# Performance work log

Hardware: AMD Instinct MI355X
Metric: run time of the kernel (lower is better)

The kernel has to match this reference:

```python
import jax, jax.numpy as jnp
import numpy as np

B, Q, C = 8, 100, 1024
H, W = 64, 64
NH = 16
HD = C // NH
SCALE = HD ** -0.5
LN_EPS = 1e-5


def setup_inputs() -> dict:
    key = jax.random.key(0)
    ks = jax.random.split(key, 8)
    xav = lambda k, shp: jax.random.normal(k, shp, jnp.float32) * (2.0 / (shp[0] + shp[-1])) ** 0.5
    return {
        "tgt": jax.random.normal(ks[0], (B, Q, C), jnp.float32),
        "memory": jax.random.normal(ks[1], (B, H, W, C), jnp.float32),
        "memory_pos_emb": jax.random.normal(ks[2], (B, H, W, C), jnp.float32),
        "query_pos_emb": jax.random.normal(ks[3], (B, Q, C), jnp.float32),
        "Wq": xav(ks[4], (C, C)),
        "Wk": xav(ks[5], (C, C)),
        "Wv": xav(ks[6], (C, C)),
        "Wo": xav(ks[7], (C, C)),
        "bo": jnp.zeros((C,), jnp.float32),
        "ln_gamma": jnp.ones((C,), jnp.float32),
        "ln_beta": jnp.zeros((C,), jnp.float32),
    }


def _layernorm(x, g, b):
    mu = jnp.mean(x, axis=-1, keepdims=True)
    var = jnp.var(x, axis=-1, keepdims=True)
    return (x - mu) * jax.lax.rsqrt(var + LN_EPS) * g + b


def reference(tgt, memory, memory_pos_emb, query_pos_emb, Wq, Wk, Wv, Wo, bo, ln_gamma, ln_beta):
    # flatten spatial dims: [B,H,W,C] -> [B,K,C]
    mem = memory.reshape(B, H * W, C)
    mpos = memory_pos_emb.reshape(B, H * W, C)
    q_in = tgt + query_pos_emb          # [B,Q,C]
    k_in = mem + mpos                    # [B,K,C]
    # projections (torch Linear: x @ W.T), split heads -> [B,nh,*,hd]
    q = (q_in @ Wq.T).reshape(B, Q, NH, HD).transpose(0, 2, 1, 3)
    k = (k_in @ Wk.T).reshape(B, -1, NH, HD).transpose(0, 2, 1, 3)
    v = (mem @ Wv.T).reshape(B, -1, NH, HD).transpose(0, 2, 1, 3)
    dots = jnp.einsum('bhid,bhjd->bhij', q, k) * SCALE   # [B,nh,Q,K]
    # slot attention: softmax over QUERY axis, then renormalize over keys
    attn = jax.nn.softmax(dots, axis=2)
    attn = attn / (jnp.sum(attn, axis=-1, keepdims=True) + 1e-8)
    updates = jnp.einsum('bhij,bhjd->bhid', attn, v)     # [B,nh,Q,hd]
    updates = updates.transpose(0, 2, 1, 3).reshape(B, Q, C)
    out = updates @ Wo.T + bo
    # residual (dropout is identity in eval) + post-LayerNorm
    return _layernorm(tgt + out, ln_gamma, ln_beta)
```

## Files before the change

kernel.cpp:

```cpp
#include <hip/hip_runtime.h>

typedef unsigned short u16;
typedef __attribute__((ext_vector_type(8))) short bf16x8;
typedef __attribute__((ext_vector_type(4))) short bf16x4;
typedef __attribute__((ext_vector_type(4))) float f32x4;
typedef __attribute__((ext_vector_type(4))) unsigned short u16x4;
typedef __attribute__((ext_vector_type(8))) unsigned short u16x8;
typedef __attribute__((ext_vector_type(4))) int i32x4;
typedef __attribute__((ext_vector_type(4))) float f4;

#define DI __device__ __forceinline__


DI u16 f2bf(float f){
  unsigned int u = __float_as_uint(f);
  return (u16)((u + 0x7FFFu + ((u >> 16) & 1u)) >> 16);
}

DI void gl_lds16(const void* g, void* l){
  __builtin_amdgcn_global_load_lds((const __attribute__((address_space(1))) unsigned int*)g,
                                   (__attribute__((address_space(3))) unsigned int*)l, 16, 0, 0);
}

__global__ __launch_bounds__(256) void prep_kv(const float* __restrict__ mem,
                                               const float* __restrict__ mpos,
                                               u16* __restrict__ kA, u16* __restrict__ vA){
  const int t = blockIdx.x * 256 + threadIdx.x;
  #pragma unroll
  for (int i = 0; i < 2; ++i){
    const size_t g = (size_t)t + (size_t)i * 2097152;
    f4 m0 = ((const f4*)mem)[g * 2];
    f4 m1 = ((const f4*)mem)[g * 2 + 1];
    f4 p0 = ((const f4*)mpos)[g * 2];
    f4 p1 = ((const f4*)mpos)[g * 2 + 1];
    u16x8 k, v;
    #pragma unroll
    for (int j = 0; j < 4; ++j){
      k[j]     = f2bf(m0[j] + p0[j]);  v[j]     = f2bf(m0[j]);
      k[j + 4] = f2bf(m1[j] + p1[j]);  v[j + 4] = f2bf(m1[j]);
    }
    ((u16x8*)kA)[g] = k;
    ((u16x8*)vA)[g] = v;
  }
}

__global__ __launch_bounds__(256) void prep_qw(const float* __restrict__ tgt,
                                               const float* __restrict__ qpos,
                                               const float* __restrict__ Wq, const float* __restrict__ Wk,
                                               const float* __restrict__ Wv, const float* __restrict__ Wo,
                                               u16* __restrict__ qA, u16* __restrict__ Wbf){
  int gid = blockIdx.x * 256 + threadIdx.x;
  const int NQ4 = 819200 / 4;
  if (gid < NQ4){
    f4 a = ((const f4*)tgt)[gid];
    f4 b = ((const f4*)qpos)[gid];
    u16x4 r;
    #pragma unroll
    for (int j = 0; j < 4; ++j) r[j] = f2bf(a[j] + b[j]);
    ((u16x4*)qA)[gid] = r;
  } else {
    int wid = gid - NQ4;
    int sel = wid >> 18;
    int off = wid & 262143;
    const float* W = (sel == 0) ? Wq : (sel == 1) ? Wk : (sel == 2) ? Wv : Wo;
    f4 w = ((const f4*)W)[off];
    u16x4 r;
    #pragma unroll
    for (int j = 0; j < 4; ++j) r[j] = f2bf(w[j]);
    ((u16x4*)(Wbf))[(size_t)sel * 262144 + off] = r;
  }
}

__global__ __launch_bounds__(512, 1) void gemm256(
    const u16* __restrict__ A, const u16* __restrict__ Bw,
    u16* __restrict__ Cb, float scale)
{
  __shared__ __align__(16) char lds[131072];
  const int tid = threadIdx.x;
  const int l = tid & 63, w = tid >> 6;
  const int nwg = gridDim.x;
  const int sbid = (blockIdx.x & 7) * (nwg >> 3) + (blockIdx.x >> 3);
  const int mb = sbid >> 2, nb = sbid & 3;
  const int m0 = mb * 256, n0 = nb * 256;
  const int fr = l & 15, fg = l >> 4;
  const int wm = w >> 2, wn = w & 3;

  char* ldsA  = lds + wm * 8192 + l * 16;
  char* ldsB  = lds + 32768 + wn * 4096 + l * 16;
  char* ldsS0 = lds + w * 1024;
  char* ldsS1 = lds + (8 + w) * 1024;
  const u16* gA0 = A  + (size_t)(m0 + w * 16 + fr) * 1024 + fg * 8;
  const u16* gA1 = A  + (size_t)(m0 + (8 + w) * 16 + fr) * 1024 + fg * 8;
  const u16* gB0 = Bw + (size_t)(n0 + w * 16 + fr) * 1024 + fg * 8;
  const u16* gB1 = Bw + (size_t)(n0 + (8 + w) * 16 + fr) * 1024 + fg * 8;

  auto stA = [&](int pp, int kh, int kt){
    const int o = kt * 64 + kh * 32;
    gl_lds16(gA0 + o, ldsS0 + pp * 65536 + kh * 16384);
    gl_lds16(gA1 + o, ldsS1 + pp * 65536 + kh * 16384);
  };
  auto stB = [&](int pp, int kh, int kt){
    const int o = kt * 64 + kh * 32;
    gl_lds16(gB0 + o, ldsS0 + pp * 65536 + 32768 + kh * 16384);
    gl_lds16(gB1 + o, ldsS1 + pp * 65536 + 32768 + kh * 16384);
  };
  auto rdA4 = [&](bf16x8* av, int pp, int kh, int mfb){
    #pragma unroll
    for (int i = 0; i < 4; ++i)
      av[i] = *(const bf16x8*)(ldsA + pp * 65536 + kh * 16384 + (mfb + i) * 1024);
  };
  auto rdB4 = [&](bf16x8* bv, int pp, int kh){
    #pragma unroll
    for (int i = 0; i < 4; ++i)
      bv[i] = *(const bf16x8*)(ldsB + pp * 65536 + kh * 16384 + i * 1024);
  };

  f32x4 acc[8][4] = {};

  stA(0, 0, 0); stB(0, 0, 0); stA(0, 1, 0); stB(0, 1, 0);
  stA(1, 0, 1); stB(1, 0, 1);
  asm volatile("s_waitcnt vmcnt(8)" ::: "memory");
  __builtin_amdgcn_s_barrier();

  auto ktbody = [&](int P, int kt){
    const int kt1 = (kt + 1 > 15) ? 15 : kt + 1;
    const int kt2 = (kt + 2 > 15) ? 15 : kt + 2;
    bf16x8 av[4], bv[4];

    rdA4(av, P, 0, 0); rdB4(bv, P, 0);
    stA(P ^ 1, 1, kt1);
    __builtin_amdgcn_s_barrier();
    __builtin_amdgcn_s_setprio(1);
    #pragma unroll
    for (int i = 0; i < 4; ++i)
      #pragma unroll
      for (int n = 0; n < 4; ++n)
        acc[i][n] = __builtin_amdgcn_mfma_f32_16x16x32_bf16(av[i], bv[n], acc[i][n], 0, 0, 0);
    __builtin_amdgcn_s_setprio(0);
    __builtin_amdgcn_s_barrier();

    rdA4(av, P, 0, 4);
    stB(P ^ 1, 1, kt1);
    asm volatile("s_waitcnt vmcnt(8)" ::: "memory");
    __builtin_amdgcn_s_barrier();
    __builtin_amdgcn_s_setprio(1);
    #pragma unroll
    for (int i = 0; i < 4; ++i)
      #pragma unroll
      for (int n = 0; n < 4; ++n)
        acc[4 + i][n] = __builtin_amdgcn_mfma_f32_16x16x32_bf16(av[i], bv[n], acc[4 + i][n], 0, 0, 0);
    __builtin_amdgcn_s_setprio(0);
    __builtin_amdgcn_s_barrier();

    rdA4(av, P, 1, 0); rdB4(bv, P, 1);
    stA(P, 0, kt2);
    __builtin_amdgcn_s_barrier();
    __builtin_amdgcn_s_setprio(1);
    #pragma unroll
    for (int i = 0; i < 4; ++i)
      #pragma unroll
      for (int n = 0; n < 4; ++n)
        acc[i][n] = __builtin_amdgcn_mfma_f32_16x16x32_bf16(av[i], bv[n], acc[i][n], 0, 0, 0);
    __builtin_amdgcn_s_setprio(0);
    __builtin_amdgcn_s_barrier();

    rdA4(av, P, 1, 4);
    stB(P, 0, kt2);
    asm volatile("s_waitcnt vmcnt(8)" ::: "memory");
    __builtin_amdgcn_s_barrier();
    __builtin_amdgcn_s_setprio(1);
    #pragma unroll
    for (int i = 0; i < 4; ++i)
      #pragma unroll
      for (int n = 0; n < 4; ++n)
        acc[4 + i][n] = __builtin_amdgcn_mfma_f32_16x16x32_bf16(av[i], bv[n], acc[4 + i][n], 0, 0, 0);
    __builtin_amdgcn_s_setprio(0);
    __builtin_amdgcn_s_barrier();
  };

  for (int kk = 0; kk < 8; ++kk){
    ktbody(0, 2 * kk);
    ktbody(1, 2 * kk + 1);
  }

  asm volatile("s_waitcnt vmcnt(0)" ::: "memory");

  #pragma unroll
  for (int mf = 0; mf < 8; ++mf){
    #pragma unroll
    for (int nf = 0; nf < 4; ++nf){
      const int gcol = n0 + wn * 64 + nf * 16 + fr;
      #pragma unroll
      for (int r = 0; r < 4; ++r){
        const int grow = m0 + wm * 128 + mf * 16 + fg * 4 + r;
        Cb[(size_t)grow * 1024 + gcol] = f2bf(acc[mf][nf][r] * scale);
      }
    }
  }
}

template<int MODE>
__global__ __launch_bounds__(256, 2) void gemm_bt(
    const u16* __restrict__ A, const u16* __restrict__ Bw,
    u16* __restrict__ Cb, float* __restrict__ Cf,
    const float* __restrict__ bias, const float* __restrict__ resid,
    int M, float scale)
{
  __shared__ u16 lA[2][128 * 32];
  __shared__ u16 lB[2][128 * 32];
  const int tid = threadIdx.x;
  const int l = tid & 63, w = tid >> 6;
  const int nwg = gridDim.x;
  int bid = blockIdx.x;
  bid = (bid & 7) * (nwg >> 3) + (bid >> 3);
  const int mb = bid >> 3, nb = bid & 7;
  const int m0 = mb * 128, n0 = nb * 128;
  const int fr = l & 15, fg = l >> 4;
  const int wr = w >> 1, wc = w & 1;

  f32x4 acc[4][4] = {};

  auto stage = [&](int buf, int kt){
    const int k0 = kt * 32;
    #pragma unroll
    for (int q = 0; q < 2; ++q){
      int r = w * 32 + q * 16 + (l >> 2);
      int ar = m0 + r; if (ar >= M) ar = M - 1;
      gl_lds16(A  + (size_t)ar * 1024 + k0 + (l & 3) * 8, &lA[buf][(w * 32 + q * 16) * 32]);
      gl_lds16(Bw + (size_t)(n0 + r) * 1024 + k0 + (l & 3) * 8, &lB[buf][(w * 32 + q * 16) * 32]);
    }
  };

  stage(0, 0);
  __syncthreads();
  for (int kt = 0; kt < 32; ++kt){
    const int cur = kt & 1;
    if (kt < 31) stage(cur ^ 1, kt + 1);
    bf16x8 av[4], bv[4];
    #pragma unroll
    for (int m = 0; m < 4; ++m)
      av[m] = *(const bf16x8*)&lA[cur][(wr * 64 + m * 16 + fr) * 32 + fg * 8];
    #pragma unroll
    for (int n = 0; n < 4; ++n)
      bv[n] = *(const bf16x8*)&lB[cur][(wc * 64 + n * 16 + fr) * 32 + fg * 8];
    #pragma unroll
    for (int m = 0; m < 4; ++m)
      #pragma unroll
      for (int n = 0; n < 4; ++n)
        acc[m][n] = __builtin_amdgcn_mfma_f32_16x16x32_bf16(av[m], bv[n], acc[m][n], 0, 0, 0);
    __syncthreads();
  }

  #pragma unroll
  for (int m = 0; m < 4; ++m){
    const int grow_base = m0 + wr * 64 + m * 16 + fg * 4;
    #pragma unroll
    for (int n = 0; n < 4; ++n){
      const int gcol = n0 + wc * 64 + n * 16 + fr;
      #pragma unroll
      for (int r = 0; r < 4; ++r){
        const int grow = grow_base + r;
        if (grow < M){
          const float v = acc[m][n][r];
          if (MODE == 0) Cb[(size_t)grow * 1024 + gcol] = f2bf(v * scale);
          else           Cf[(size_t)grow * 1024 + gcol] = v + bias[gcol] + resid[(size_t)grow * 1024 + gcol];
        }
      }
    }
  }
}

__global__ __launch_bounds__(64, 1) void attn_k(
    const u16* __restrict__ qp, const u16* __restrict__ kp, const u16* __restrict__ vp,
    float* __restrict__ updpart, float* __restrict__ rspart)
{
  const int bidx = blockIdx.x;
  const int c = bidx & 7, h = (bidx >> 3) & 15, b = bidx >> 7;
  const int bh = b * 16 + h;
  const int l = threadIdx.x;
  const int fr = l & 15, fg = l >> 4;

  __shared__ u16 qlds[112 * 64];
  for (int t = 0; t < 14; ++t){
    int chunk = t * 64 + l;
    int row = chunk >> 3, cb = chunk & 7;
    i32x4 val = {0, 0, 0, 0};
    if (row < 100)
      val = *(const i32x4*)(qp + (size_t)(b * 100 + row) * 1024 + h * 64 + cb * 8);
    *(i32x4*)((char*)qlds + row * 128 + ((cb ^ (row & 7)) * 16)) = val;
  }
  __syncthreads();

  bf16x8 qf[7][2];
  #pragma unroll
  for (int n = 0; n < 7; ++n)
    #pragma unroll
    for (int ks = 0; ks < 2; ++ks){
      int row = n * 16 + fr;
      int cb = ks * 4 + fg;
      qf[n][ks] = *(const bf16x8*)((const char*)qlds + row * 128 + ((cb ^ (row & 7)) * 16));
    }

  f32x4 acc[7][4] = {};
  float rs[7] = {};
  const f32x4 fz = {0.f, 0.f, 0.f, 0.f};
  const size_t kvbase = ((size_t)b * 4096) * 1024 + h * 64;

  for (int t = 0; t < 32; ++t){
    const int j0 = c * 512 + t * 16;
    bf16x8 kf0 = *(const bf16x8*)(kp + kvbase + (size_t)(j0 + fr) * 1024 + fg * 8);
    bf16x8 kf1 = *(const bf16x8*)(kp + kvbase + (size_t)(j0 + fr) * 1024 + 32 + fg * 8);
    f32x4 s[7];
    #pragma unroll
    for (int n = 0; n < 7; ++n){
      s[n] = __builtin_amdgcn_mfma_f32_16x16x32_bf16(kf0, qf[n][0], fz, 0, 0, 0);
      s[n] = __builtin_amdgcn_mfma_f32_16x16x32_bf16(kf1, qf[n][1], s[n], 0, 0, 0);
    }
    if (fr >= 4){ s[6][0] = -1e30f; s[6][1] = -1e30f; s[6][2] = -1e30f; s[6][3] = -1e30f; }

    float pv[7][4];
    #pragma unroll
    for (int r = 0; r < 4; ++r){
      float m = s[0][r];
      #pragma unroll
      for (int n = 1; n < 7; ++n) m = fmaxf(m, s[n][r]);
      m = fmaxf(m, __shfl_xor(m, 1)); m = fmaxf(m, __shfl_xor(m, 2));
      m = fmaxf(m, __shfl_xor(m, 4)); m = fmaxf(m, __shfl_xor(m, 8));
      float sum = 0.f;
      #pragma unroll
      for (int n = 0; n < 7; ++n){ float e = __expf(s[n][r] - m); pv[n][r] = e; sum += e; }
      sum += __shfl_xor(sum, 1); sum += __shfl_xor(sum, 2);
      sum += __shfl_xor(sum, 4); sum += __shfl_xor(sum, 8);
      float inv = 1.0f / sum;
      #pragma unroll
      for (int n = 0; n < 7; ++n) pv[n][r] *= inv;
    }

    bf16x4 pk[7];
    #pragma unroll
    for (int n = 0; n < 7; ++n){
      rs[n] += pv[n][0] + pv[n][1] + pv[n][2] + pv[n][3];
      bf16x4 t4;
      t4[0] = (short)f2bf(pv[n][0]); t4[1] = (short)f2bf(pv[n][1]);
      t4[2] = (short)f2bf(pv[n][2]); t4[3] = (short)f2bf(pv[n][3]);
      pk[n] = t4;
    }

    bf16x4 vf[4];
    #pragma unroll
    for (int dt = 0; dt < 4; ++dt){
      bf16x4 tv;
      #pragma unroll
      for (int jj = 0; jj < 4; ++jj)
        tv[jj] = (short)vp[kvbase + (size_t)(j0 + fg * 4 + jj) * 1024 + dt * 16 + fr];
      vf[dt] = tv;
    }

    #pragma unroll
    for (int n = 0; n < 7; ++n)
      #pragma unroll
      for (int dt = 0; dt < 4; ++dt)
        acc[n][dt] = __builtin_amdgcn_mfma_f32_16x16x16bf16_1k(vf[dt], pk[n], acc[n][dt], 0, 0, 0);
  }

  #pragma unroll
  for (int n = 0; n < 7; ++n){
    float v = rs[n];
    v += __shfl_xor(v, 16); v += __shfl_xor(v, 32);
    if (l < 16) rspart[((size_t)c * 128 + bh) * 112 + n * 16 + l] = v;
  }
  float* ub = updpart + ((size_t)c * 128 + bh) * 64 * 112;
  #pragma unroll
  for (int n = 0; n < 7; ++n)
    #pragma unroll
    for (int dt = 0; dt < 4; ++dt)
      #pragma unroll
      for (int r = 0; r < 4; ++r){
        int d = dt * 16 + fg * 4 + r;
        int i = n * 16 + fr;
        ub[d * 112 + i] = acc[n][dt][r];
      }
}

__global__ __launch_bounds__(256) void nrm_k(const float* __restrict__ updpart,
                                             const float* __restrict__ rspart,
                                             u16* __restrict__ updn){
  int gid = blockIdx.x * 256 + threadIdx.x;
  int b = gid / 102400;
  int rem = gid % 102400;
  int i = rem / 1024;
  int cc = rem & 1023;
  int h = cc >> 6, d = cc & 63;
  int bh = b * 16 + h;
  float sum = 0.f, rsum = 0.f;
  #pragma unroll
  for (int c = 0; c < 8; ++c){
    sum  += updpart[(((size_t)c * 128 + bh) * 64 + d) * 112 + i];
    rsum += rspart[((size_t)c * 128 + bh) * 112 + i];
  }
  updn[gid] = f2bf(sum / (rsum + 1e-8f));
}

__global__ __launch_bounds__(256) void ln_k(const float* __restrict__ x,
                                            const float* __restrict__ g,
                                            const float* __restrict__ be,
                                            float* __restrict__ out){
  const int row = blockIdx.x;
  const int tid = threadIdx.x;
  const f4 xv = *(const f4*)(x + (size_t)row * 1024 + tid * 4);
  float s = xv[0] + xv[1] + xv[2] + xv[3];
  float q = xv[0]*xv[0] + xv[1]*xv[1] + xv[2]*xv[2] + xv[3]*xv[3];
  #pragma unroll
  for (int m = 1; m < 64; m <<= 1){ s += __shfl_xor(s, m); q += __shfl_xor(q, m); }
  __shared__ float ss[4], qq[4];
  const int w = tid >> 6;
  if ((tid & 63) == 0){ ss[w] = s; qq[w] = q; }
  __syncthreads();
  s = ss[0] + ss[1] + ss[2] + ss[3];
  q = qq[0] + qq[1] + qq[2] + qq[3];
  const float mu = s * (1.0f / 1024.0f);
  const float var = q * (1.0f / 1024.0f) - mu * mu;
  const float rstd = rsqrtf(var + 1e-5f);
  const f4 gv = *(const f4*)(g + tid * 4);
  const f4 bv = *(const f4*)(be + tid * 4);
  f4 o;
  #pragma unroll
  for (int j = 0; j < 4; ++j) o[j] = (xv[j] - mu) * rstd * gv[j] + bv[j];
  *(f4*)(out + (size_t)row * 1024 + tid * 4) = o;
}

extern "C" void kernel_launch(void* const* d_in, const int* in_sizes, int n_in,
                              void* d_out, int out_size, void* d_ws, size_t ws_size,
                              hipStream_t stream)
{
  const float* tgt   = (const float*)d_in[0];
  const float* mem   = (const float*)d_in[1];
  const float* mpos  = (const float*)d_in[2];
  const float* qpos  = (const float*)d_in[3];
  const float* Wq    = (const float*)d_in[4];
  const float* Wk    = (const float*)d_in[5];
  const float* Wv    = (const float*)d_in[6];
  const float* Wo    = (const float*)d_in[7];
  const float* bo    = (const float*)d_in[8];
  const float* gamma = (const float*)d_in[9];
  const float* beta  = (const float*)d_in[10];

  char* ws = (char*)d_ws;
  u16* qA     = (u16*)(ws + 0);
  u16* Wbf    = (u16*)(ws + 1638400);
  u16* kA     = (u16*)(ws + 10027008);
  u16* vA     = (u16*)(ws + 77135872);
  u16* qproj  = (u16*)(ws + 144244736);
  u16* kproj  = (u16*)(ws + 145883136);
  u16* vproj  = kA;
  float* updpart = (float*)(ws + 77135872);
  float* rspart  = (float*)(ws + 77135872 + 29360128);
  u16*   updn    = (u16*)  (ws + 77135872 + 29818880);
  float* resid   = (float*)(ws + 77135872 + 31457280);

  prep_kv<<<8192, 256, 0, stream>>>(mem, mpos, kA, vA);
  prep_qw<<<4896, 256, 0, stream>>>(tgt, qpos, Wq, Wk, Wv, Wo, qA, Wbf);
  gemm_bt<0><<<56,  256, 0, stream>>>(qA, Wbf, qproj, nullptr, nullptr, nullptr, 800, 0.125f);
  gemm256<<<512, 512, 0, stream>>>(kA, Wbf + 1048576, kproj, 1.0f);
  gemm256<<<512, 512, 0, stream>>>(vA, Wbf + 2097152, vproj, 1.0f);
  attn_k<<<1024, 64, 0, stream>>>(qproj, kproj, vproj, updpart, rspart);
  nrm_k<<<3200, 256, 0, stream>>>(updpart, rspart, updn);
  gemm_bt<1><<<56, 256, 0, stream>>>(updn, Wbf + 3145728, nullptr, resid, bo, tgt, 800, 1.0f);
  ln_k<<<800, 256, 0, stream>>>(resid, gamma, beta, (float*)d_out);
}
```

Before: 402.0 us.

## Prefetch K/V tiles into registers and LDS in attention, coalesce norm and prep

The attention kernel now prefetches the next 16-row K tile into registers and stages the next V tile through a double-buffered LDS area with coalesced 16-byte loads, instead of issuing scalar strided global loads for V on every iteration. The aim is to hide global load latency behind the MFMA work and cut the many small uncoalesced V loads. The normalization kernel is remapped so each block covers one (b,h,d) with the query index on threads, so the strided updpart reads become contiguous. prep_kv processes four elements per thread with nontemporal loads to cut streaming cache pollution. Costs are extra registers, extra LDS, and 12 idle threads per norm block.

Result: faster. 369.7 us (-8.0%).

```diff
diff --git a/kernel.cpp b/kernel.cpp
--- a/kernel.cpp
+++ b/kernel.cpp
@@ -27,12 +27,12 @@
                                                u16* __restrict__ kA, u16* __restrict__ vA){
   const int t = blockIdx.x * 256 + threadIdx.x;
   #pragma unroll
-  for (int i = 0; i < 2; ++i){
-    const size_t g = (size_t)t + (size_t)i * 2097152;
-    f4 m0 = ((const f4*)mem)[g * 2];
-    f4 m1 = ((const f4*)mem)[g * 2 + 1];
-    f4 p0 = ((const f4*)mpos)[g * 2];
-    f4 p1 = ((const f4*)mpos)[g * 2 + 1];
+  for (int i = 0; i < 4; ++i){
+    const size_t g = (size_t)t + (size_t)i * 1048576;
+    f4 m0 = __builtin_nontemporal_load((const f4*)mem  + g * 2);
+    f4 m1 = __builtin_nontemporal_load((const f4*)mem  + g * 2 + 1);
+    f4 p0 = __builtin_nontemporal_load((const f4*)mpos + g * 2);
+    f4 p1 = __builtin_nontemporal_load((const f4*)mpos + g * 2 + 1);
     u16x8 k, v;
     #pragma unroll
     for (int j = 0; j < 4; ++j){
@@ -281,6 +281,8 @@
   const int fr = l & 15, fg = l >> 4;
 
   __shared__ u16 qlds[112 * 64];
+  __shared__ __align__(16) u16 vlds[2][16 * 64];
+
   for (int t = 0; t < 14; ++t){
     int chunk = t * 64 + l;
     int row = chunk >> 3, cb = chunk & 7;
@@ -305,16 +307,43 @@
   float rs[7] = {};
   const f32x4 fz = {0.f, 0.f, 0.f, 0.f};
   const size_t kvbase = ((size_t)b * 4096) * 1024 + h * 64;
+  const int j00 = c * 512;
+
+  const u16* ksrc = kp + kvbase + (size_t)fr * 1024 + fg * 8;
+  const u16* vsrc = vp + kvbase + (size_t)(l >> 3) * 1024 + (l & 7) * 8;
+
+  auto loadK = [&](int t, bf16x8& k0, bf16x8& k1){
+    const size_t ro = (size_t)(j00 + t * 16) * 1024;
+    k0 = *(const bf16x8*)(ksrc + ro);
+    k1 = *(const bf16x8*)(ksrc + ro + 32);
+  };
+  auto loadV = [&](int t, bf16x8& a, bf16x8& bb){
+    const size_t ro = (size_t)(j00 + t * 16) * 1024;
+    a  = *(const bf16x8*)(vsrc + ro);
+    bb = *(const bf16x8*)(vsrc + ro + 8 * 1024);
+  };
+  auto writeV = [&](int buf, bf16x8 a, bf16x8 bb){
+    *(bf16x8*)&vlds[buf][l * 8] = a;
+    *(bf16x8*)&vlds[buf][512 + l * 8] = bb;
+  };
+
+  bf16x8 kc0, kc1, kn0, kn1, vn0, vn1;
+  loadK(0, kc0, kc1);
+  loadV(0, vn0, vn1);
+  writeV(0, vn0, vn1);
 
   for (int t = 0; t < 32; ++t){
-    const int j0 = c * 512 + t * 16;
-    bf16x8 kf0 = *(const bf16x8*)(kp + kvbase + (size_t)(j0 + fr) * 1024 + fg * 8);
-    bf16x8 kf1 = *(const bf16x8*)(kp + kvbase + (size_t)(j0 + fr) * 1024 + 32 + fg * 8);
+    const int cur = t & 1;
+    if (t < 31){
+      loadK(t + 1, kn0, kn1);
+      loadV(t + 1, vn0, vn1);
+    }
+
     f32x4 s[7];
     #pragma unroll
     for (int n = 0; n < 7; ++n){
-      s[n] = __builtin_amdgcn_mfma_f32_16x16x32_bf16(kf0, qf[n][0], fz, 0, 0, 0);
-      s[n] = __builtin_amdgcn_mfma_f32_16x16x32_bf16(kf1, qf[n][1], s[n], 0, 0, 0);
+      s[n] = __builtin_amdgcn_mfma_f32_16x16x32_bf16(kc0, qf[n][0], fz, 0, 0, 0);
+      s[n] = __builtin_amdgcn_mfma_f32_16x16x32_bf16(kc1, qf[n][1], s[n], 0, 0, 0);
     }
     if (fr >= 4){ s[6][0] = -1e30f; s[6][1] = -1e30f; s[6][2] = -1e30f; s[6][3] = -1e30f; }
 
@@ -352,7 +381,7 @@
       bf16x4 tv;
       #pragma unroll
       for (int jj = 0; jj < 4; ++jj)
-        tv[jj] = (short)vp[kvbase + (size_t)(j0 + fg * 4 + jj) * 1024 + dt * 16 + fr];
+        tv[jj] = (short)vlds[cur][(fg * 4 + jj) * 64 + dt * 16 + fr];
       vf[dt] = tv;
     }
 
@@ -361,6 +390,11 @@
       #pragma unroll
       for (int dt = 0; dt < 4; ++dt)
         acc[n][dt] = __builtin_amdgcn_mfma_f32_16x16x16bf16_1k(vf[dt], pk[n], acc[n][dt], 0, 0, 0);
+
+    if (t < 31){
+      writeV(cur ^ 1, vn0, vn1);
+      kc0 = kn0; kc1 = kn1;
+    }
   }
 
   #pragma unroll
@@ -382,23 +416,22 @@
       }
 }
 
-__global__ __launch_bounds__(256) void nrm_k(const float* __restrict__ updpart,
+__global__ __launch_bounds__(128) void nrm_k(const float* __restrict__ updpart,
                                              const float* __restrict__ rspart,
                                              u16* __restrict__ updn){
-  int gid = blockIdx.x * 256 + threadIdx.x;
-  int b = gid / 102400;
-  int rem = gid % 102400;
-  int i = rem / 1024;
-  int cc = rem & 1023;
-  int h = cc >> 6, d = cc & 63;
-  int bh = b * 16 + h;
+  const int bid = blockIdx.x;
+  const int d = bid & 63, h = (bid >> 6) & 15, b = bid >> 10;
+  const int bh = b * 16 + h;
+  const int tid = threadIdx.x;
+  const int i = (tid < 112) ? tid : 111;
   float sum = 0.f, rsum = 0.f;
   #pragma unroll
-  for (int c = 0; c < 8; ++c){
-    sum  += updpart[(((size_t)c * 128 + bh) * 64 + d) * 112 + i];
-    rsum += rspart[((size_t)c * 128 + bh) * 112 + i];
-  }
-  updn[gid] = f2bf(sum / (rsum + 1e-8f));
+  for (int cc = 0; cc < 8; ++cc){
+    sum  += updpart[(((size_t)cc * 128 + bh) * 64 + d) * 112 + i];
+    rsum += rspart[((size_t)cc * 128 + bh) * 112 + i];
+  }
+  if (tid < 100)
+    updn[((size_t)b * 100 + tid) * 1024 + h * 64 + d] = f2bf(sum / (rsum + 1e-8f));
 }
 
 __global__ __launch_bounds__(256) void ln_k(const float* __restrict__ x,
@@ -458,13 +491,13 @@
   u16*   updn    = (u16*)  (ws + 77135872 + 29818880);
   float* resid   = (float*)(ws + 77135872 + 31457280);
 
-  prep_kv<<<8192, 256, 0, stream>>>(mem, mpos, kA, vA);
+  prep_kv<<<4096, 256, 0, stream>>>(mem, mpos, kA, vA);
   prep_qw<<<4896, 256, 0, stream>>>(tgt, qpos, Wq, Wk, Wv, Wo, qA, Wbf);
   gemm_bt<0><<<56,  256, 0, stream>>>(qA, Wbf, qproj, nullptr, nullptr, nullptr, 800, 0.125f);
   gemm256<<<512, 512, 0, stream>>>(kA, Wbf + 1048576, kproj, 1.0f);
   gemm256<<<512, 512, 0, stream>>>(vA, Wbf + 2097152, vproj, 1.0f);
   attn_k<<<1024, 64, 0, stream>>>(qproj, kproj, vproj, updpart, rspart);
-  nrm_k<<<3200, 256, 0, stream>>>(updpart, rspart, updn);
+  nrm_k<<<8192, 128, 0, stream>>>(updpart, rspart, updn);
   gemm_bt<1><<<56, 256, 0, stream>>>(updn, Wbf + 3145728, nullptr, resid, bo, tgt, 800, 1.0f);
   ln_k<<<800, 256, 0, stream>>>(resid, gamma, beta, (float*)d_out);
 }
```
